# Performance work log

Measured on AMD Instinct MI355X. Metric: run time of the kernel, lower is better.

Reference implementation:

```python
import jax, jax.numpy as jnp
import numpy as np

NEG_FILL = -1000.0

def setup_inputs() -> dict:
    key = jax.random.key(0)
    k1, k2, k3, k4 = jax.random.split(key, 4)
    B, N, D = 16, 2048, 64
    q = jax.random.normal(k1, (B, N, D), dtype=jnp.float32)
    k = jax.random.normal(k2, (B, N, D), dtype=jnp.float32)
    v = jax.random.normal(k3, (B, N, D), dtype=jnp.float32)
    mask = jax.random.randint(k4, (B, N, N), 0, 2) == 1
    return {"q": q, "k": k, "v": v, "mask": mask}

def reference(q, k, v, mask):
    # Faithful to the torch module: scale by sqrt(seq_len) = len(q[0])**0.5,
    # masked positions set to -1000.0, softmax over dim=1 (NOT the last dim).
    seq_len = q.shape[1]
    scores = jnp.einsum('bnd,bmd->bnm', q, k) / jnp.sqrt(jnp.float32(seq_len))
    scores = jnp.where(mask, NEG_FILL, scores)
    attn = jax.nn.softmax(scores, axis=1)  # dim=1 as in nn.Softmax(dim=1)
    out = jnp.einsum('bnm,bmd->bnd', attn, v)
    return out
```

## Files before the change

### kernel.cpp

```cpp
#include <hip/hip_runtime.h>
#include <hip/hip_bf16.h>


#define B_ 16
#define N_ 2048
#define D_ 64
#define SCALE 0.022097086912079608f
#define MCH 2
#define SNCH 4
#define NWORD (N_ / 32)

typedef __attribute__((ext_vector_type(8))) short bf16x8;
typedef __attribute__((ext_vector_type(4))) float f32x4;

static __device__ __forceinline__ short f2bf(float x) {
  unsigned u = __float_as_uint(x);
  return (short)((u + 0x7FFF + ((u >> 16) & 1)) >> 16);
}

static __device__ __forceinline__ bf16x8 load8(const short* p) {
  return *reinterpret_cast<const bf16x8*>(p);
}

static __device__ __forceinline__ bf16x8 load8f(const float* p) {
  const f32x4 a = *reinterpret_cast<const f32x4*>(p);
  const f32x4 b = *reinterpret_cast<const f32x4*>(p + 4);
  bf16x8 r;
  r[0] = f2bf(a[0]); r[1] = f2bf(a[1]); r[2] = f2bf(a[2]); r[3] = f2bf(a[3]);
  r[4] = f2bf(b[0]); r[5] = f2bf(b[1]); r[6] = f2bf(b[2]); r[7] = f2bf(b[3]);
  return r;
}

__global__ __launch_bounds__(256) void prep_kernel(
    const float* __restrict__ q, const float* __restrict__ k,
    const int* __restrict__ mask, short* __restrict__ qb,
    short* __restrict__ kb, unsigned* __restrict__ bits) {
  if (blockIdx.y == 0) {
    const size_t w = (size_t)blockIdx.x * 256 + threadIdx.x;
    const int4* p = reinterpret_cast<const int4*>(mask) + w * 8;
    unsigned r = 0;
#pragma unroll
    for (int j = 0; j < 8; ++j) {
      const int4 x = p[j];
      r |= (x.x ? 1u : 0u) << (j * 4);
      r |= (x.y ? 1u : 0u) << (j * 4 + 1);
      r |= (x.z ? 1u : 0u) << (j * 4 + 2);
      r |= (x.w ? 1u : 0u) << (j * 4 + 3);
    }
    bits[w] = r;
  } else {
    if (blockIdx.x >= (B_ * N_ * D_) / (256 * 8)) return;
    const size_t i = ((size_t)blockIdx.x * 256 + threadIdx.x) * 8;
    const float* src = (blockIdx.y == 2) ? k : q;
    short* dst = (blockIdx.y == 2) ? kb : qb;
    *reinterpret_cast<bf16x8*>(dst + i) = load8f(src + i);
  }
}

__global__ __launch_bounds__(256) void score_kernel(
    const short* __restrict__ qb, const short* __restrict__ kb,
    const unsigned* __restrict__ bits, short* __restrict__ pstore,
    float* __restrict__ csp) {
  const int b = blockIdx.x;
  const int wave = threadIdx.x >> 6;
  const int lane = threadIdx.x & 63;
  const int l15 = lane & 15;
  const int lhi = lane >> 4;
  const int n0 = blockIdx.y * 64 + wave * 16;
  const int n16 = blockIdx.y * 4 + wave;
  const int mbase = blockIdx.z * (N_ / SNCH);

  const short* qbb = qb + (size_t)b * N_ * D_;
  const short* kbb = kb + (size_t)b * N_ * D_;
  const unsigned* bitsb = bits + (size_t)b * N_ * NWORD;
  float* cspb = csp + ((size_t)b * 128 + n16) * N_;
  short* psb = pstore + (((size_t)b * 128 + n16) * 64) * 512;

  const bf16x8 qf0 = load8(qbb + (n0 + l15) * D_ + lhi * 8);
  const bf16x8 qf1 = load8(qbb + (n0 + l15) * D_ + 32 + lhi * 8);

  __shared__ __align__(16) short pbuf[4][16][72];
  __shared__ float csl[4][512];

#pragma unroll
  for (int j = 0; j < 8; ++j) csl[wave][j * 64 + lane] = 0.f;

  for (int m0 = mbase; m0 < mbase + N_ / SNCH; m0 += 64) {
    uint2 w2[4];
#pragma unroll
    for (int r = 0; r < 4; ++r)
      w2[r] = *reinterpret_cast<const uint2*>(
          bitsb + (size_t)(n0 + lhi * 4 + r) * NWORD + (m0 >> 5));
#pragma unroll
    for (int cg = 0; cg < 4; ++cg) {
      const int mc = m0 + cg * 16;
      const bf16x8 kf0 = load8(kbb + (mc + l15) * D_ + lhi * 8);
      const bf16x8 kf1 = load8(kbb + (mc + l15) * D_ + 32 + lhi * 8);
      f32x4 acc = {0.f, 0.f, 0.f, 0.f};
      acc = __builtin_amdgcn_mfma_f32_16x16x32_bf16(qf0, kf0, acc, 0, 0, 0);
      acc = __builtin_amdgcn_mfma_f32_16x16x32_bf16(qf1, kf1, acc, 0, 0, 0);
      float cp = 0.f;
#pragma unroll
      for (int r = 0; r < 4; ++r) {
        const unsigned wsel = (cg < 2) ? w2[r].x : w2[r].y;
        const unsigned bit = (wsel >> ((cg & 1) * 16 + l15)) & 1u;
        const float p = bit ? 0.f : __expf(acc[r] * SCALE);
        cp += p;
        pbuf[wave][lhi * 4 + r][cg * 16 + l15] = f2bf(p);
      }
      cp += __shfl_xor(cp, 16, 64);
      cp += __shfl_xor(cp, 32, 64);
      if (lane < 16) csl[wave][m0 - mbase + cg * 16 + l15] += cp;
    }
    __builtin_amdgcn_wave_barrier();
    const bf16x8 pa0 =
        *reinterpret_cast<const bf16x8*>(&pbuf[wave][l15][lhi * 8]);
    const bf16x8 pa1 =
        *reinterpret_cast<const bf16x8*>(&pbuf[wave][l15][32 + lhi * 8]);
    *reinterpret_cast<bf16x8*>(psb + (size_t)(m0 >> 5) * 512 + lane * 8) = pa0;
    *reinterpret_cast<bf16x8*>(psb + (size_t)((m0 >> 5) + 1) * 512 + lane * 8) =
        pa1;
    __builtin_amdgcn_wave_barrier();
  }

  __builtin_amdgcn_wave_barrier();
#pragma unroll
  for (int j = 0; j < 2; ++j) {
    f32x4 cv;
#pragma unroll
    for (int e = 0; e < 4; ++e) cv[e] = csl[wave][lane * 8 + j * 4 + e];
    *reinterpret_cast<f32x4*>(cspb + mbase + lane * 8 + j * 4) = cv;
  }
}

__global__ __launch_bounds__(256) void vprep_kernel(
    const float* __restrict__ v, const float* __restrict__ csp,
    short* __restrict__ vt) {
  const int b = blockIdx.x;
  const int m0 = blockIdx.y * 64;
  const int tid = threadIdx.x;
  __shared__ float csl[4][64];
  __shared__ float cst[64];
  __shared__ float lds[64][65];

  {
    const int col = m0 + (tid & 63);
    const int q4 = tid >> 6;
    float s = 0.f;
    for (int j = 0; j < 32; ++j)
      s += csp[((size_t)b * 128 + q4 * 32 + j) * N_ + col];
    csl[q4][tid & 63] = s;
  }
  __syncthreads();
  if (tid < 64) cst[tid] = csl[0][tid] + csl[1][tid] + csl[2][tid] + csl[3][tid];
  __syncthreads();

  const float* vb = v + (size_t)b * N_ * D_;
#pragma unroll
  for (int pass = 0; pass < 4; ++pass) {
    const int mloc = pass * 16 + (tid >> 4);
    const int d4 = (tid & 15) * 4;
    const f32x4 x = *reinterpret_cast<const f32x4*>(vb + (m0 + mloc) * D_ + d4);
    const float ic = 1.0f / cst[mloc];
    lds[mloc][d4 + 0] = x[0] * ic;
    lds[mloc][d4 + 1] = x[1] * ic;
    lds[mloc][d4 + 2] = x[2] * ic;
    lds[mloc][d4 + 3] = x[3] * ic;
  }
  __syncthreads();
  const int d = tid >> 2;
  const int seg = tid & 3;
  bf16x8 o0, o1;
#pragma unroll
  for (int i = 0; i < 8; ++i) o0[i] = f2bf(lds[seg * 16 + i][d]);
#pragma unroll
  for (int i = 0; i < 8; ++i) o1[i] = f2bf(lds[seg * 16 + 8 + i][d]);
  short* dst = vt + (size_t)b * D_ * N_ + (size_t)d * N_ + m0 + seg * 16;
  *reinterpret_cast<bf16x8*>(dst) = o0;
  *reinterpret_cast<bf16x8*>(dst + 8) = o1;
}

__global__ __launch_bounds__(256) void pv_kernel(const short* __restrict__ pstore,
                                                 const short* __restrict__ vt,
                                                 float* __restrict__ outp) {
  const int b = blockIdx.x;
  const int wave = threadIdx.x >> 6;
  const int lane = threadIdx.x & 63;
  const int l15 = lane & 15;
  const int lhi = lane >> 4;
  const int n0 = blockIdx.y * 64 + wave * 16;
  const int n16 = blockIdx.y * 4 + wave;
  const int mibase = blockIdx.z * (64 / MCH);

  const short* psb =
      pstore + (((size_t)b * 128 + n16) * 64) * 512 + (size_t)lane * 8;
  const short* vtb = vt + (size_t)b * D_ * N_;

  f32x4 oacc[4];
#pragma unroll
  for (int d = 0; d < 4; ++d) oacc[d] = (f32x4){0.f, 0.f, 0.f, 0.f};

#pragma unroll 2
  for (int mi = mibase; mi < mibase + 64 / MCH; ++mi) {
    const bf16x8 pa = load8(psb + (size_t)mi * 512);
    const int m0 = mi * 32;
#pragma unroll
    for (int dsub = 0; dsub < 4; ++dsub) {
      const bf16x8 vf =
          load8(vtb + (size_t)(dsub * 16 + l15) * N_ + m0 + lhi * 8);
      oacc[dsub] =
          __builtin_amdgcn_mfma_f32_16x16x32_bf16(pa, vf, oacc[dsub], 0, 0, 0);
    }
  }

  float* dst = outp + (size_t)blockIdx.z * B_ * N_ * D_ + (size_t)b * N_ * D_;
#pragma unroll
  for (int dsub = 0; dsub < 4; ++dsub)
#pragma unroll
    for (int r = 0; r < 4; ++r)
      dst[(size_t)(n0 + lhi * 4 + r) * D_ + dsub * 16 + l15] = oacc[dsub][r];
}

__global__ __launch_bounds__(256) void reduce_out(const float* __restrict__ outp,
                                                  float* __restrict__ out) {
  const size_t i = ((size_t)blockIdx.x * 256 + threadIdx.x) * 4;
  f32x4 s = *reinterpret_cast<const f32x4*>(outp + i);
#pragma unroll
  for (int z = 1; z < MCH; ++z) {
    const f32x4 x =
        *reinterpret_cast<const f32x4*>(outp + (size_t)z * B_ * N_ * D_ + i);
    s[0] += x[0]; s[1] += x[1]; s[2] += x[2]; s[3] += x[3];
  }
  *reinterpret_cast<f32x4*>(out + i) = s;
}

__global__ __launch_bounds__(256) void colsum_fb(
    const float* __restrict__ q, const float* __restrict__ k,
    const int* __restrict__ mask, float* __restrict__ colsum) {
  const int b = blockIdx.x;
  const int wave = threadIdx.x >> 6;
  const int lane = threadIdx.x & 63;
  const int l15 = lane & 15;
  const int lhi = lane >> 4;
  const int m0 = blockIdx.y * 64 + wave * 16;
  const float* qbp = q + (size_t)b * N_ * D_;
  const float* kbp = k + (size_t)b * N_ * D_;
  const int* maskb = mask + (size_t)b * N_ * N_;
  const bf16x8 kf0 = load8f(kbp + (m0 + l15) * D_ + lhi * 8);
  const bf16x8 kf1 = load8f(kbp + (m0 + l15) * D_ + 32 + lhi * 8);
  float partial = 0.f;
  for (int n0 = 0; n0 < N_; n0 += 16) {
    bf16x8 qf0 = load8f(qbp + (n0 + l15) * D_ + lhi * 8);
    bf16x8 qf1 = load8f(qbp + (n0 + l15) * D_ + 32 + lhi * 8);
    f32x4 acc = {0.f, 0.f, 0.f, 0.f};
    acc = __builtin_amdgcn_mfma_f32_16x16x32_bf16(qf0, kf0, acc, 0, 0, 0);
    acc = __builtin_amdgcn_mfma_f32_16x16x32_bf16(qf1, kf1, acc, 0, 0, 0);
#pragma unroll
    for (int r = 0; r < 4; ++r) {
      const int n = n0 + lhi * 4 + r;
      partial +=
          maskb[(size_t)n * N_ + m0 + l15] ? 0.f : __expf(acc[r] * SCALE);
    }
  }
  partial += __shfl_xor(partial, 16, 64);
  partial += __shfl_xor(partial, 32, 64);
  if (lane < 16) colsum[(size_t)b * N_ + m0 + l15] = partial;
}

__global__ __launch_bounds__(256) void attn_out_fb(
    const float* __restrict__ q, const float* __restrict__ k,
    const float* __restrict__ v, const int* __restrict__ mask,
    const float* __restrict__ colsum, float* __restrict__ out) {
  const int b = blockIdx.x;
  const int wave = threadIdx.x >> 6;
  const int lane = threadIdx.x & 63;
  const int l15 = lane & 15;
  const int lhi = lane >> 4;
  const int n0 = blockIdx.y * 64 + wave * 16;
  const float* qbp = q + (size_t)b * N_ * D_;
  const float* kbp = k + (size_t)b * N_ * D_;
  const float* vbp = v + (size_t)b * N_ * D_;
  const int* maskb = mask + (size_t)b * N_ * N_;
  const float* csb = colsum + (size_t)b * N_;
  const bf16x8 qf0 = load8f(qbp + (n0 + l15) * D_ + lhi * 8);
  const bf16x8 qf1 = load8f(qbp + (n0 + l15) * D_ + 32 + lhi * 8);
  __shared__ __align__(16) short pbuf[4][16][32];
  f32x4 oacc[4];
#pragma unroll
  for (int d = 0; d < 4; ++d) oacc[d] = (f32x4){0.f, 0.f, 0.f, 0.f};
  for (int m0 = 0; m0 < N_; m0 += 32) {
#pragma unroll
    for (int cg = 0; cg < 2; ++cg) {
      const int mc = m0 + cg * 16;
      bf16x8 kf0 = load8f(kbp + (mc + l15) * D_ + lhi * 8);
      bf16x8 kf1 = load8f(kbp + (mc + l15) * D_ + 32 + lhi * 8);
      f32x4 acc = {0.f, 0.f, 0.f, 0.f};
      acc = __builtin_amdgcn_mfma_f32_16x16x32_bf16(qf0, kf0, acc, 0, 0, 0);
      acc = __builtin_amdgcn_mfma_f32_16x16x32_bf16(qf1, kf1, acc, 0, 0, 0);
      const float ic = 1.0f / csb[mc + l15];
#pragma unroll
      for (int r = 0; r < 4; ++r) {
        const int n = n0 + lhi * 4 + r;
        const float p = maskb[(size_t)n * N_ + mc + l15]
                            ? 0.f
                            : __expf(acc[r] * SCALE) * ic;
        pbuf[wave][lhi * 4 + r][cg * 16 + l15] = f2bf(p);
      }
    }
    __syncthreads();
    const bf16x8 pa =
        *reinterpret_cast<const bf16x8*>(&pbuf[wave][l15][lhi * 8]);
#pragma unroll
    for (int dsub = 0; dsub < 4; ++dsub) {
      bf16x8 vf;
#pragma unroll
      for (int j = 0; j < 8; ++j)
        vf[j] = f2bf(vbp[(m0 + lhi * 8 + j) * D_ + dsub * 16 + l15]);
      oacc[dsub] =
          __builtin_amdgcn_mfma_f32_16x16x32_bf16(pa, vf, oacc[dsub], 0, 0, 0);
    }
    __syncthreads();
  }
#pragma unroll
  for (int dsub = 0; dsub < 4; ++dsub)
#pragma unroll
    for (int r = 0; r < 4; ++r)
      out[(size_t)b * N_ * D_ + (size_t)(n0 + lhi * 4 + r) * D_ + dsub * 16 +
          l15] = oacc[dsub][r];
}

extern "C" void kernel_launch(void* const* d_in, const int* in_sizes, int n_in,
                              void* d_out, int out_size, void* d_ws,
                              size_t ws_size, hipStream_t stream) {
  const float* q = (const float*)d_in[0];
  const float* k = (const float*)d_in[1];
  const float* v = (const float*)d_in[2];
  const int* mask = (const int*)d_in[3];
  float* out = (float*)d_out;

  const size_t MB = 1024 * 1024;
  const size_t qb_off = 0;
  const size_t kb_off = qb_off + 4 * MB;
  const size_t vt_off = kb_off + 4 * MB;
  const size_t bt_off = vt_off + 4 * MB;
  const size_t cs_off = bt_off + 8 * MB;
  const size_t ps_off = cs_off + 16 * MB;
  const size_t op_off = ps_off + 128 * MB;
  const size_t need = op_off + (size_t)MCH * B_ * N_ * D_ * 4;

  if (ws_size >= need) {
    short* qbf = (short*)((char*)d_ws + qb_off);
    short* kbf = (short*)((char*)d_ws + kb_off);
    short* vt = (short*)((char*)d_ws + vt_off);
    unsigned* bits = (unsigned*)((char*)d_ws + bt_off);
    float* csp = (float*)((char*)d_ws + cs_off);
    short* pstore = (short*)((char*)d_ws + ps_off);
    float* outp = (float*)((char*)d_ws + op_off);

    prep_kernel<<<dim3(8192, 3), 256, 0, stream>>>(q, k, mask, qbf, kbf, bits);
    score_kernel<<<dim3(B_, N_ / 64, SNCH), 256, 0, stream>>>(qbf, kbf, bits,
                                                              pstore, csp);
    vprep_kernel<<<dim3(B_, N_ / 64), 256, 0, stream>>>(v, csp, vt);
    pv_kernel<<<dim3(B_, N_ / 64, MCH), 256, 0, stream>>>(pstore, vt, outp);
    reduce_out<<<(B_ * N_ * D_) / (256 * 4), 256, 0, stream>>>(outp, out);
  } else {
    float* colsum = (float*)d_ws;
    colsum_fb<<<dim3(B_, N_ / 64), 256, 0, stream>>>(q, k, mask, colsum);
    attn_out_fb<<<dim3(B_, N_ / 64), 256, 0, stream>>>(q, k, v, mask, colsum,
                                                       out);
  }
}
```

Before: 519.6 us.

## Recompute scores in PV kernel instead of storing bf16 probability matrix

The score pass no longer writes the full bf16 exp(score) matrix to global memory and only accumulates column sums. A new fused output kernel recomputes QK^T, applies the mask and exp, stages P through LDS, and multiplies by the scaled transposed V directly. This removes a 128 MB write and read of the probability matrix. In exchange the QK^T matmul and exp work are done twice.

```diff
diff --git a/kernel.cpp b/kernel.cpp
--- a/kernel.cpp
+++ b/kernel.cpp
@@ -57,10 +57,9 @@
   }
 }
 
-__global__ __launch_bounds__(256) void score_kernel(
+__global__ __launch_bounds__(256) void colsum_kernel(
     const short* __restrict__ qb, const short* __restrict__ kb,
-    const unsigned* __restrict__ bits, short* __restrict__ pstore,
-    float* __restrict__ csp) {
+    const unsigned* __restrict__ bits, float* __restrict__ csp) {
   const int b = blockIdx.x;
   const int wave = threadIdx.x >> 6;
   const int lane = threadIdx.x & 63;
@@ -74,14 +73,11 @@
   const short* kbb = kb + (size_t)b * N_ * D_;
   const unsigned* bitsb = bits + (size_t)b * N_ * NWORD;
   float* cspb = csp + ((size_t)b * 128 + n16) * N_;
-  short* psb = pstore + (((size_t)b * 128 + n16) * 64) * 512;
 
   const bf16x8 qf0 = load8(qbb + (n0 + l15) * D_ + lhi * 8);
   const bf16x8 qf1 = load8(qbb + (n0 + l15) * D_ + 32 + lhi * 8);
 
-  __shared__ __align__(16) short pbuf[4][16][72];
   __shared__ float csl[4][512];
-
 #pragma unroll
   for (int j = 0; j < 8; ++j) csl[wave][j * 64 + lane] = 0.f;
 
@@ -104,25 +100,13 @@
       for (int r = 0; r < 4; ++r) {
         const unsigned wsel = (cg < 2) ? w2[r].x : w2[r].y;
         const unsigned bit = (wsel >> ((cg & 1) * 16 + l15)) & 1u;
-        const float p = bit ? 0.f : __expf(acc[r] * SCALE);
-        cp += p;
-        pbuf[wave][lhi * 4 + r][cg * 16 + l15] = f2bf(p);
+        cp += bit ? 0.f : __expf(acc[r] * SCALE);
       }
       cp += __shfl_xor(cp, 16, 64);
       cp += __shfl_xor(cp, 32, 64);
       if (lane < 16) csl[wave][m0 - mbase + cg * 16 + l15] += cp;
     }
-    __builtin_amdgcn_wave_barrier();
-    const bf16x8 pa0 =
-        *reinterpret_cast<const bf16x8*>(&pbuf[wave][l15][lhi * 8]);
-    const bf16x8 pa1 =
-        *reinterpret_cast<const bf16x8*>(&pbuf[wave][l15][32 + lhi * 8]);
-    *reinterpret_cast<bf16x8*>(psb + (size_t)(m0 >> 5) * 512 + lane * 8) = pa0;
-    *reinterpret_cast<bf16x8*>(psb + (size_t)((m0 >> 5) + 1) * 512 + lane * 8) =
-        pa1;
-    __builtin_amdgcn_wave_barrier();
-  }
-
+  }
   __builtin_amdgcn_wave_barrier();
 #pragma unroll
   for (int j = 0; j < 2; ++j) {
@@ -180,37 +164,72 @@
   *reinterpret_cast<bf16x8*>(dst + 8) = o1;
 }
 
-__global__ __launch_bounds__(256) void pv_kernel(const short* __restrict__ pstore,
-                                                 const short* __restrict__ vt,
-                                                 float* __restrict__ outp) {
+__global__ __launch_bounds__(256) void fused_out_kernel(
+    const short* __restrict__ qb, const short* __restrict__ kb,
+    const short* __restrict__ vt, const unsigned* __restrict__ bits,
+    float* __restrict__ outp) {
   const int b = blockIdx.x;
   const int wave = threadIdx.x >> 6;
   const int lane = threadIdx.x & 63;
   const int l15 = lane & 15;
   const int lhi = lane >> 4;
   const int n0 = blockIdx.y * 64 + wave * 16;
-  const int n16 = blockIdx.y * 4 + wave;
-  const int mibase = blockIdx.z * (64 / MCH);
-
-  const short* psb =
-      pstore + (((size_t)b * 128 + n16) * 64) * 512 + (size_t)lane * 8;
+  const int mbase = blockIdx.z * (N_ / MCH);
+
+  const short* qbb = qb + (size_t)b * N_ * D_;
+  const short* kbb = kb + (size_t)b * N_ * D_;
   const short* vtb = vt + (size_t)b * D_ * N_;
+  const unsigned* bitsb = bits + (size_t)b * N_ * NWORD;
+
+  const bf16x8 qf0 = load8(qbb + (n0 + l15) * D_ + lhi * 8);
+  const bf16x8 qf1 = load8(qbb + (n0 + l15) * D_ + 32 + lhi * 8);
+
+  __shared__ __align__(16) short pbuf[4][16][72];
 
   f32x4 oacc[4];
 #pragma unroll
   for (int d = 0; d < 4; ++d) oacc[d] = (f32x4){0.f, 0.f, 0.f, 0.f};
 
-#pragma unroll 2
-  for (int mi = mibase; mi < mibase + 64 / MCH; ++mi) {
-    const bf16x8 pa = load8(psb + (size_t)mi * 512);
-    const int m0 = mi * 32;
-#pragma unroll
-    for (int dsub = 0; dsub < 4; ++dsub) {
-      const bf16x8 vf =
-          load8(vtb + (size_t)(dsub * 16 + l15) * N_ + m0 + lhi * 8);
-      oacc[dsub] =
-          __builtin_amdgcn_mfma_f32_16x16x32_bf16(pa, vf, oacc[dsub], 0, 0, 0);
-    }
+  for (int m0 = mbase; m0 < mbase + N_ / MCH; m0 += 64) {
+    uint2 w2[4];
+#pragma unroll
+    for (int r = 0; r < 4; ++r)
+      w2[r] = *reinterpret_cast<const uint2*>(
+          bitsb + (size_t)(n0 + lhi * 4 + r) * NWORD + (m0 >> 5));
+#pragma unroll
+    for (int cg = 0; cg < 4; ++cg) {
+      const int mc = m0 + cg * 16;
+      const bf16x8 kf0 = load8(kbb + (mc + l15) * D_ + lhi * 8);
+      const bf16x8 kf1 = load8(kbb + (mc + l15) * D_ + 32 + lhi * 8);
+      f32x4 acc = {0.f, 0.f, 0.f, 0.f};
+      acc = __builtin_amdgcn_mfma_f32_16x16x32_bf16(qf0, kf0, acc, 0, 0, 0);
+      acc = __builtin_amdgcn_mfma_f32_16x16x32_bf16(qf1, kf1, acc, 0, 0, 0);
+#pragma unroll
+      for (int r = 0; r < 4; ++r) {
+        const unsigned wsel = (cg < 2) ? w2[r].x : w2[r].y;
+        const unsigned bit = (wsel >> ((cg & 1) * 16 + l15)) & 1u;
+        const float p = bit ? 0.f : __expf(acc[r] * SCALE);
+        pbuf[wave][lhi * 4 + r][cg * 16 + l15] = f2bf(p);
+      }
+    }
+    __builtin_amdgcn_wave_barrier();
+    const bf16x8 pa0 =
+        *reinterpret_cast<const bf16x8*>(&pbuf[wave][l15][lhi * 8]);
+    const bf16x8 pa1 =
+        *reinterpret_cast<const bf16x8*>(&pbuf[wave][l15][32 + lhi * 8]);
+#pragma unroll
+    for (int half = 0; half < 2; ++half) {
+      const bf16x8 pa = half ? pa1 : pa0;
+      const int mh = m0 + half * 32;
+#pragma unroll
+      for (int dsub = 0; dsub < 4; ++dsub) {
+        const bf16x8 vf =
+            load8(vtb + (size_t)(dsub * 16 + l15) * N_ + mh + lhi * 8);
+        oacc[dsub] =
+            __builtin_amdgcn_mfma_f32_16x16x32_bf16(pa, vf, oacc[dsub], 0, 0, 0);
+      }
+    }
+    __builtin_amdgcn_wave_barrier();
   }
 
   float* dst = outp + (size_t)blockIdx.z * B_ * N_ * D_ + (size_t)b * N_ * D_;
@@ -344,8 +363,7 @@
   const size_t vt_off = kb_off + 4 * MB;
   const size_t bt_off = vt_off + 4 * MB;
   const size_t cs_off = bt_off + 8 * MB;
-  const size_t ps_off = cs_off + 16 * MB;
-  const size_t op_off = ps_off + 128 * MB;
+  const size_t op_off = cs_off + 16 * MB;
   const size_t need = op_off + (size_t)MCH * B_ * N_ * D_ * 4;
 
   if (ws_size >= need) {
@@ -354,14 +372,14 @@
     short* vt = (short*)((char*)d_ws + vt_off);
     unsigned* bits = (unsigned*)((char*)d_ws + bt_off);
     float* csp = (float*)((char*)d_ws + cs_off);
-    short* pstore = (short*)((char*)d_ws + ps_off);
     float* outp = (float*)((char*)d_ws + op_off);
 
     prep_kernel<<<dim3(8192, 3), 256, 0, stream>>>(q, k, mask, qbf, kbf, bits);
-    score_kernel<<<dim3(B_, N_ / 64, SNCH), 256, 0, stream>>>(qbf, kbf, bits,
-                                                              pstore, csp);
+    colsum_kernel<<<dim3(B_, N_ / 64, SNCH), 256, 0, stream>>>(qbf, kbf, bits,
+                                                               csp);
     vprep_kernel<<<dim3(B_, N_ / 64), 256, 0, stream>>>(v, csp, vt);
-    pv_kernel<<<dim3(B_, N_ / 64, MCH), 256, 0, stream>>>(pstore, vt, outp);
+    fused_out_kernel<<<dim3(B_, N_ / 64, MCH), 256, 0, stream>>>(qbf, kbf, vt,
+                                                                 bits, outp);
     reduce_out<<<(B_ * N_ * D_) / (256 * 4), 256, 0, stream>>>(outp, out);
   } else {
     float* colsum = (float*)d_ws;
```

New measurement: 574.3 us. +10.5%, slower.
